# Kernel tuning notes

Hardware: AMD Instinct MI355X
Metric: run time of the kernel (lower is better)

The kernel has to match this reference:

```python
import jax, jax.numpy as jnp
import numpy as np

B, N, H, ITERS = 4, 4096, 128, 8
EPS = 1e-5  # torch LayerNorm default


def _mlp(x, w1, b1, w2, b2, w3, b3):
    x = jax.nn.relu(x @ w1.T + b1)
    x = jax.nn.relu(x @ w2.T + b2)
    return x @ w3.T + b3


def setup_inputs() -> dict:
    key = jax.random.key(0)
    ks = jax.random.split(key, 16)
    s = 0.05
    nrm = lambda k, shape: jax.random.normal(k, shape, jnp.float32) * s
    z = lambda *shape: jnp.zeros(shape, jnp.float32)
    return {
        "x": jax.random.normal(ks[0], (B, N, N), jnp.float32),
        "k": jax.random.uniform(ks[1], (B,), jnp.float32, 1.0, 10.0),
        "n": jax.random.uniform(ks[2], (B,), jnp.float32, 10.0, 100.0),
        "mask": (jax.random.uniform(ks[3], (B, N)) < 0.9).astype(jnp.float32),
        # init MLP: 2 -> H -> H -> H (torch Linear convention: [out, in])
        "init_w1": nrm(ks[4], (H, 2)), "init_b1": z(H),
        "init_w2": nrm(ks[5], (H, H)), "init_b2": z(H),
        "init_w3": nrm(ks[6], (H, H)), "init_b3": z(H),
        # msg MLP: H -> H -> H -> H
        "msg_w1": nrm(ks[7], (H, H)), "msg_b1": z(H),
        "msg_w2": nrm(ks[8], (H, H)), "msg_b2": z(H),
        "msg_w3": nrm(ks[9], (H, H)), "msg_b3": z(H),
        # LSTMCell (gate order i, f, g, o)
        "lstm_wih": nrm(ks[10], (4 * H, H)), "lstm_whh": nrm(ks[11], (4 * H, H)),
        "lstm_bih": z(4 * H), "lstm_bhh": z(4 * H),
        # LayerNorm affine
        "ln_g": jnp.ones(H, jnp.float32), "ln_b": z(H),
        # vote MLP: H -> H -> H -> 1
        "vote_w1": nrm(ks[12], (H, H)), "vote_b1": z(H),
        "vote_w2": nrm(ks[13], (H, H)), "vote_b2": z(H),
        "vote_w3": nrm(ks[14], (1, H)), "vote_b3": z(1),
    }


def reference(x, k, n, mask,
              init_w1, init_b1, init_w2, init_b2, init_w3, init_b3,
              msg_w1, msg_b1, msg_w2, msg_b2, msg_w3, msg_b3,
              lstm_wih, lstm_whh, lstm_bih, lstm_bhh,
              ln_g, ln_b,
              vote_w1, vote_b1, vote_w2, vote_b2, vote_w3, vote_b3):
    b, n_node, _ = x.shape

    def ln(h):
        mu = h.mean(-1, keepdims=True)
        xc = h - mu
        var = (xc * xc).mean(-1, keepdims=True)
        return xc * jax.lax.rsqrt(var + EPS) * ln_g + ln_b

    nk = jnp.stack([k, n], axis=1)                          # [B, 2]
    init0 = _mlp(nk, init_w1, init_b1, init_w2, init_b2, init_w3, init_b3)
    h = jnp.broadcast_to(init0[:, None, :], (b, n_node, init0.shape[-1]))  # [B, N, H]
    c = jnp.zeros_like(h)
    embed = ln(h)
    for _ in range(ITERS):
        m = _mlp(embed, msg_w1, msg_b1, msg_w2, msg_b2, msg_w3, msg_b3)   # [B, N, H]
        msg = jnp.einsum('bij,bjh->bih', x, m)                            # dense aggregation
        gates = msg @ lstm_wih.T + lstm_bih + h @ lstm_whh.T + lstm_bhh   # [B, N, 4H]
        i, f, g, o = jnp.split(gates, 4, axis=-1)
        c = jax.nn.sigmoid(f) * c + jax.nn.sigmoid(i) * jnp.tanh(g)
        h = jax.nn.sigmoid(o) * jnp.tanh(c)
        embed = ln(h)
    vote = _mlp(embed, vote_w1, vote_b1, vote_w2, vote_b2, vote_w3, vote_b3)[..., 0]  # [B, N]
    return jax.nn.sigmoid((vote * mask).sum(axis=1))        # [B]
```

## Files before the change

kernel.cpp:

```cpp
#include <hip/hip_runtime.h>
#include <cstddef>
#include <cstdint>

#define LN_EPS 1e-5f

typedef __attribute__((ext_vector_type(8))) short bf16x8;
typedef __attribute__((ext_vector_type(4))) float f32x4;

__device__ __forceinline__ unsigned short f2bf(float f) {
    unsigned u = __float_as_uint(f);
    u += 0x7FFFu + ((u >> 16) & 1u);
    return (unsigned short)(u >> 16);
}
__device__ __forceinline__ float bf2f(unsigned short s) {
    return __uint_as_float(((unsigned)s) << 16);
}
__device__ __forceinline__ float sigf(float x) { return 1.f / (1.f + __expf(-x)); }

__device__ __forceinline__ void gload_lds16(const void* g, void* l) {
    __builtin_amdgcn_global_load_lds(
        (const __attribute__((address_space(1))) unsigned int*)(unsigned long long)(uintptr_t)g,
        (__attribute__((address_space(3))) unsigned int*)(unsigned int)(uintptr_t)l,
        16, 0, 0);
}

__device__ __forceinline__ void layer128(const unsigned short* __restrict__ W,
                                         const bf16x8 a[4], f32x4 acc[8],
                                         int lr, int lq)
{
#pragma unroll
    for (int s = 0; s < 4; ++s) {
#pragma unroll
        for (int tn = 0; tn < 8; ++tn) {
            bf16x8 b = *(const bf16x8*)(W + (tn * 16 + lr) * 128 + s * 32 + lq * 8);
            acc[tn] = __builtin_amdgcn_mfma_f32_16x16x32_bf16(a[s], b, acc[tn], 0, 0, 0);
        }
    }
}

template<bool FP8>
__global__ __launch_bounds__(256)
void msg_mlp_kernel(const unsigned short* __restrict__ embed,
                    const unsigned short* __restrict__ w1, const float* __restrict__ b1,
                    const unsigned short* __restrict__ w2, const float* __restrict__ b2,
                    const unsigned short* __restrict__ w3, const float* __restrict__ b3,
                    unsigned short* __restrict__ m_t, unsigned char* __restrict__ m8,
                    int N)
{
    __shared__ unsigned short sact[4][16][136];
    const int lane = threadIdx.x & 63, wave = threadIdx.x >> 6;
    const int lr = lane & 15, lq = lane >> 4;
    const int r0 = (blockIdx.x * 4 + wave) * 16;

    bf16x8 a[4];
    f32x4 acc[8];

#pragma unroll
    for (int s = 0; s < 4; ++s)
        a[s] = *(const bf16x8*)(embed + (long long)(r0 + lr) * 128 + s * 32 + lq * 8);
#pragma unroll
    for (int tn = 0; tn < 8; ++tn) acc[tn] = (f32x4)(0.f);
    layer128(w1, a, acc, lr, lq);

#pragma unroll
    for (int tn = 0; tn < 8; ++tn) {
        float bb = b1[tn * 16 + lr];
#pragma unroll
        for (int r = 0; r < 4; ++r) {
            float v = acc[tn][r] + bb; v = v > 0.f ? v : 0.f;
            sact[wave][lq * 4 + r][tn * 16 + lr] = f2bf(v);
        }
    }
    __syncthreads();
#pragma unroll
    for (int s = 0; s < 4; ++s)
        a[s] = *(const bf16x8*)&sact[wave][lr][s * 32 + lq * 8];
#pragma unroll
    for (int tn = 0; tn < 8; ++tn) acc[tn] = (f32x4)(0.f);
    layer128(w2, a, acc, lr, lq);

#pragma unroll
    for (int tn = 0; tn < 8; ++tn) {
        float bb = b2[tn * 16 + lr];
#pragma unroll
        for (int r = 0; r < 4; ++r) {
            float v = acc[tn][r] + bb; v = v > 0.f ? v : 0.f;
            sact[wave][lq * 4 + r][tn * 16 + lr] = f2bf(v);
        }
    }
    __syncthreads();
#pragma unroll
    for (int s = 0; s < 4; ++s)
        a[s] = *(const bf16x8*)&sact[wave][lr][s * 32 + lq * 8];
#pragma unroll
    for (int tn = 0; tn < 8; ++tn) acc[tn] = (f32x4)(0.f);
    layer128(w3, a, acc, lr, lq);

    const int batch = r0 / N;
    const int rin0 = r0 - batch * N + lq * 4;
#pragma unroll
    for (int tn = 0; tn < 8; ++tn) {
        float bb = b3[tn * 16 + lr];
        float v0 = acc[tn][0] + bb, v1 = acc[tn][1] + bb;
        float v2 = acc[tn][2] + bb, v3 = acc[tn][3] + bb;
        if constexpr (FP8) {
            int pk = __builtin_amdgcn_cvt_pk_fp8_f32(v0, v1, 0, false);
            pk = __builtin_amdgcn_cvt_pk_fp8_f32(v2, v3, pk, true);
            *(unsigned int*)(m8 + (long long)(batch * 128 + tn * 16 + lr) * N + rin0) = (unsigned)pk;
        } else {
            ushort4 o;
            o.x = f2bf(v0); o.y = f2bf(v1); o.z = f2bf(v2); o.w = f2bf(v3);
            *(ushort4*)(m_t + ((long long)(batch * 128 + tn * 16 + lr)) * N + rin0) = o;
        }
    }
}

__global__ __launch_bounds__(256)
void agg_fp8_kernel(const unsigned char* __restrict__ x8,
                    const unsigned char* __restrict__ m8,
                    unsigned short* __restrict__ msgp, int N, long long BNH)
{
    __shared__ unsigned char sA[2][128 * 128];
    __shared__ unsigned char sB[2][128 * 128];

    const int tid = threadIdx.x;
    const int lane = tid & 63, w = tid >> 6;
    const int lr = lane & 15, lq = lane >> 4;
    const int wr = w & 1, wc = w >> 1;
    const int r0 = blockIdx.x * 128;
    const int ksp = blockIdx.y;
    const int batch = blockIdx.z;
    const int kbase = ksp * (N >> 2);
    const int nsteps = (N >> 2) >> 7;

    const unsigned char* xrow = x8 + (long long)batch * N * N;
    const unsigned char* mrow = m8 + (long long)batch * 128 * N;

    f32x4 acc[4][4];
#pragma unroll
    for (int tr = 0; tr < 4; ++tr)
#pragma unroll
        for (int tn = 0; tn < 4; ++tn) acc[tr][tn] = (f32x4)(0.f);

    auto stage = [&](int b, int step) {
        const int k0 = kbase + step * 128;
#pragma unroll
        for (int j = 0; j < 4; ++j) {
            const int c = ((w * 4 + j) << 6) + lane;
            const int row = c >> 3;
            const int gs = (c & 7) ^ (row & 7);
            gload_lds16(xrow + (long long)(r0 + row) * N + k0 + gs * 16,
                        (char*)sA[b] + (w * 4 + j) * 1024);
        }
#pragma unroll
        for (int j = 0; j < 4; ++j) {
            const int c = ((w * 4 + j) << 6) + lane;
            const int row = c >> 3;
            const int gs = (c & 7) ^ (row & 7);
            gload_lds16(mrow + (long long)row * N + k0 + gs * 16,
                        (char*)sB[b] + (w * 4 + j) * 1024);
        }
    };

    stage(0, 0);
    __syncthreads();
    int buf = 0;
    for (int step = 0; step < nsteps; ++step) {
        if (step + 1 < nsteps) stage(buf ^ 1, step + 1);
        const unsigned char* A  = sA[buf];
        const unsigned char* Bp = sB[buf];
#pragma unroll
        for (int ks = 0; ks < 4; ++ks) {
            const int g    = ks * 4 + lq;
            const int half = (g & 1) << 3;
            const int s16  = g >> 1;
            long af[4], bfr[4];
#pragma unroll
            for (int tr = 0; tr < 4; ++tr) {
                const int row = wr * 64 + tr * 16 + lr;
                af[tr] = *(const long*)(A + row * 128 + ((s16 ^ (row & 7)) << 4) + half);
            }
#pragma unroll
            for (int tn = 0; tn < 4; ++tn) {
                const int row = wc * 64 + tn * 16 + lr;
                bfr[tn] = *(const long*)(Bp + row * 128 + ((s16 ^ (row & 7)) << 4) + half);
            }
#pragma unroll
            for (int tr = 0; tr < 4; ++tr)
#pragma unroll
                for (int tn = 0; tn < 4; ++tn)
                    acc[tr][tn] = __builtin_amdgcn_mfma_f32_16x16x32_fp8_fp8(
                        af[tr], bfr[tn], acc[tr][tn], 0, 0, 0);
        }
        __syncthreads();
        buf ^= 1;
    }

    unsigned short* outb = msgp + (long long)ksp * BNH + (long long)(batch * N + r0) * 128;
#pragma unroll
    for (int tr = 0; tr < 4; ++tr)
#pragma unroll
        for (int tn = 0; tn < 4; ++tn)
#pragma unroll
            for (int r = 0; r < 4; ++r)
                outb[(long long)(wr * 64 + tr * 16 + lq * 4 + r) * 128 + wc * 64 + tn * 16 + lr]
                    = f2bf(acc[tr][tn][r]);
}

__global__ __launch_bounds__(256)
void agg_fallback_kernel(const float* __restrict__ xf,
                         const unsigned short* __restrict__ mt, float* __restrict__ msgp0,
                         int N)
{
    __shared__ float sacc[4][16][132];
    const int lane = threadIdx.x & 63, wave = threadIdx.x >> 6;
    const int lr = lane & 15, lq = lane >> 4;
    const int batch = blockIdx.y;
    const int rowBase = blockIdx.x * 16;
    const int kBase = wave * (N >> 2);
    const int kIters = N >> 7;

    const float* af = xf + (long long)batch * N * N + (long long)(rowBase + lr) * N + kBase + lq * 8;
    const long long bbase = (long long)batch * 128 * N + (long long)lr * N + kBase + lq * 8;

    f32x4 acc[8];
#pragma unroll
    for (int tn = 0; tn < 8; ++tn) acc[tn] = (f32x4)(0.f);

    for (int it = 0; it < kIters; ++it) {
        const int k = it * 32;
        float4 lo = *(const float4*)(af + k);
        float4 hi = *(const float4*)(af + k + 4);
        bf16x8 a0;
        a0[0] = (short)f2bf(lo.x); a0[1] = (short)f2bf(lo.y);
        a0[2] = (short)f2bf(lo.z); a0[3] = (short)f2bf(lo.w);
        a0[4] = (short)f2bf(hi.x); a0[5] = (short)f2bf(hi.y);
        a0[6] = (short)f2bf(hi.z); a0[7] = (short)f2bf(hi.w);
#pragma unroll
        for (int tn = 0; tn < 8; ++tn) {
            bf16x8 b0 = *(const bf16x8*)(mt + bbase + (long long)tn * 16 * N + k);
            acc[tn] = __builtin_amdgcn_mfma_f32_16x16x32_bf16(a0, b0, acc[tn], 0, 0, 0);
        }
    }

#pragma unroll
    for (int tn = 0; tn < 8; ++tn)
#pragma unroll
        for (int r = 0; r < 4; ++r)
            sacc[wave][lq * 4 + r][tn * 16 + lr] = acc[tn][r];
    __syncthreads();
    {
        const int t = threadIdx.x;
        const int row = t >> 4, cb2 = (t & 15) * 8;
        float o[8];
#pragma unroll
        for (int j = 0; j < 8; ++j)
            o[j] = sacc[0][row][cb2 + j] + sacc[1][row][cb2 + j]
                 + sacc[2][row][cb2 + j] + sacc[3][row][cb2 + j];
        float* dst = msgp0 + (long long)(batch * N + rowBase + row) * 128 + cb2;
        *(float4*)dst = make_float4(o[0], o[1], o[2], o[3]);
        *(float4*)(dst + 4) = make_float4(o[4], o[5], o[6], o[7]);
    }
}

template<int NPART, bool BF16P>
__global__ __launch_bounds__(256)
void gates_lstm_kernel(const void* __restrict__ msgp, long long BNH,
                       unsigned short* hb, float* cb,
                       const unsigned short* __restrict__ wih,
                       const unsigned short* __restrict__ whh,
                       const float* __restrict__ bih, const float* __restrict__ bhh,
                       const float* __restrict__ lng, const float* __restrict__ lnb,
                       unsigned short* __restrict__ embed_out)
{
    __shared__ float sred[4][16][2];
    const int lane = threadIdx.x & 63, wave = threadIdx.x >> 6;
    const int lr = lane & 15, lq = lane >> 4;
    const int r0 = blockIdx.x * 16;

    f32x4 acc[8];
#pragma unroll
    for (int t = 0; t < 8; ++t) acc[t] = (f32x4)(0.f);

    bf16x8 a[4];
#pragma unroll
    for (int s = 0; s < 4; ++s) {
        const long long base = (long long)(r0 + lr) * 128 + s * 32 + lq * 8;
        float v[8];
        if constexpr (BF16P) {
            const unsigned short* mp = (const unsigned short*)msgp;
            bf16x8 t0 = *(const bf16x8*)(mp + base);
#pragma unroll
            for (int e = 0; e < 8; ++e) v[e] = bf2f((unsigned short)t0[e]);
#pragma unroll
            for (int j = 1; j < NPART; ++j) {
                bf16x8 tj = *(const bf16x8*)(mp + (long long)j * BNH + base);
#pragma unroll
                for (int e = 0; e < 8; ++e) v[e] += bf2f((unsigned short)tj[e]);
            }
        } else {
            const float* mp = (const float*)msgp;
            float4 t0 = *(const float4*)(mp + base);
            float4 t1 = *(const float4*)(mp + base + 4);
            v[0] = t0.x; v[1] = t0.y; v[2] = t0.z; v[3] = t0.w;
            v[4] = t1.x; v[5] = t1.y; v[6] = t1.z; v[7] = t1.w;
#pragma unroll
            for (int j = 1; j < NPART; ++j) {
                float4 u0 = *(const float4*)(mp + (long long)j * BNH + base);
                float4 u1 = *(const float4*)(mp + (long long)j * BNH + base + 4);
                v[0] += u0.x; v[1] += u0.y; v[2] += u0.z; v[3] += u0.w;
                v[4] += u1.x; v[5] += u1.y; v[6] += u1.z; v[7] += u1.w;
            }
        }
        bf16x8 r8;
#pragma unroll
        for (int e = 0; e < 8; ++e) r8[e] = (short)f2bf(v[e]);
        a[s] = r8;
    }
#pragma unroll
    for (int s = 0; s < 4; ++s)
#pragma unroll
        for (int tt = 0; tt < 8; ++tt) {
            const int brow = (tt >> 1) * 128 + wave * 32 + (tt & 1) * 16 + lr;
            bf16x8 b = *(const bf16x8*)(wih + brow * 128 + s * 32 + lq * 8);
            acc[tt] = __builtin_amdgcn_mfma_f32_16x16x32_bf16(a[s], b, acc[tt], 0, 0, 0);
        }
#pragma unroll
    for (int s = 0; s < 4; ++s)
        a[s] = *(const bf16x8*)((const unsigned short*)hb + (long long)(r0 + lr) * 128 + s * 32 + lq * 8);
#pragma unroll
    for (int s = 0; s < 4; ++s)
#pragma unroll
        for (int tt = 0; tt < 8; ++tt) {
            const int brow = (tt >> 1) * 128 + wave * 32 + (tt & 1) * 16 + lr;
            bf16x8 b = *(const bf16x8*)(whh + brow * 128 + s * 32 + lq * 8);
            acc[tt] = __builtin_amdgcn_mfma_f32_16x16x32_bf16(a[s], b, acc[tt], 0, 0, 0);
        }

    float hn[2][4];
    float4* cw = (float4*)cb;
#pragma unroll
    for (int half = 0; half < 2; ++half) {
        const int col = wave * 32 + half * 16 + lr;
        const float bi  = bih[col]       + bhh[col];
        const float bf_ = bih[col + 128] + bhh[col + 128];
        const float bg  = bih[col + 256] + bhh[col + 256];
        const float bo  = bih[col + 384] + bhh[col + 384];
        const long long cidx = ((long long)blockIdx.x * 8 + wave * 2 + half) * 64 + lane;
        float4 cold = cw[cidx];
        float co[4] = {cold.x, cold.y, cold.z, cold.w};
        float cn[4];
#pragma unroll
        for (int r = 0; r < 4; ++r) {
            float iv = acc[0 + half][r] + bi;
            float fv = acc[2 + half][r] + bf_;
            float gv = acc[4 + half][r] + bg;
            float ov = acc[6 + half][r] + bo;
            float cc = sigf(fv) * co[r] + sigf(iv) * tanhf(gv);
            cn[r] = cc;
            hn[half][r] = sigf(ov) * tanhf(cc);
        }
        float4 cnew = {cn[0], cn[1], cn[2], cn[3]};
        cw[cidx] = cnew;
    }

    float ps1[4], ps2[4];
#pragma unroll
    for (int r = 0; r < 4; ++r) {
        float s1 = hn[0][r] + hn[1][r];
        float s2 = hn[0][r] * hn[0][r] + hn[1][r] * hn[1][r];
#pragma unroll
        for (int m = 1; m <= 8; m <<= 1) {
            s1 += __shfl_xor(s1, m);
            s2 += __shfl_xor(s2, m);
        }
        ps1[r] = s1; ps2[r] = s2;
    }
    if (lr == 0) {
#pragma unroll
        for (int r = 0; r < 4; ++r) {
            sred[wave][lq * 4 + r][0] = ps1[r];
            sred[wave][lq * 4 + r][1] = ps2[r];
        }
    }
    __syncthreads();

#pragma unroll
    for (int half = 0; half < 2; ++half) {
        const int col = wave * 32 + half * 16 + lr;
        const float g = lng[col], bb = lnb[col];
#pragma unroll
        for (int r = 0; r < 4; ++r) {
            const int row = lq * 4 + r;
            float S1 = sred[0][row][0] + sred[1][row][0] + sred[2][row][0] + sred[3][row][0];
            float S2 = sred[0][row][1] + sred[1][row][1] + sred[2][row][1] + sred[3][row][1];
            float mean = S1 * (1.f / 128.f);
// ... 92 lines not shown
    float h2 = b2[j];
    for (int q = 0; q < H; ++q) h2 += w2[j * H + q] * s1[q];
    h2 = h2 > 0.f ? h2 : 0.f;
    s2[j] = h2; __syncthreads();
    float o = b3[j];
    for (int q = 0; q < H; ++q) o += w3[j * H + q] * s2[q];
    init0[b * H + j] = o;

    red[j] = o; __syncthreads();
    for (int s = 64; s > 0; s >>= 1) { if (j < s) red[j] += red[j + s]; __syncthreads(); }
    float mu = red[0] / (float)H;
    __syncthreads();
    float d = o - mu;
    red[j] = d * d; __syncthreads();
    for (int s = 64; s > 0; s >>= 1) { if (j < s) red[j] += red[j + s]; __syncthreads(); }
    float var = red[0] / (float)H;
    embed0[b * H + j] = d * rsqrtf(var + LN_EPS) * lng[j] + lnb[j];
}

__global__ void bcast_kernel(const float* __restrict__ init0, const float* __restrict__ embed0,
                             unsigned short* __restrict__ hb, float* __restrict__ cb,
                             unsigned short* __restrict__ embed,
                             long long total, long long NH)
{
    long long idx = (long long)blockIdx.x * blockDim.x + threadIdx.x;
    if (idx >= total) return;
    int b = (int)(idx / NH);
    int j = (int)(idx & 127);
    hb[idx] = f2bf(init0[b * 128 + j]);
    embed[idx] = f2bf(embed0[b * 128 + j]);
    cb[idx] = 0.f;
}

__global__ void cast8_kernel(const float* __restrict__ x, unsigned char* __restrict__ x8,
                             long long n8)
{
    long long i = ((long long)blockIdx.x * blockDim.x + threadIdx.x);
    if (i >= n8) return;
    const float* s = x + i * 8;
    float4 a = *(const float4*)s;
    float4 b = *(const float4*)(s + 4);
    int lo = __builtin_amdgcn_cvt_pk_fp8_f32(a.x, a.y, 0, false);
    lo = __builtin_amdgcn_cvt_pk_fp8_f32(a.z, a.w, lo, true);
    int hi = __builtin_amdgcn_cvt_pk_fp8_f32(b.x, b.y, 0, false);
    hi = __builtin_amdgcn_cvt_pk_fp8_f32(b.z, b.w, hi, true);
    int2 o; o.x = lo; o.y = hi;
    *(int2*)(x8 + i * 8) = o;
}

struct CastArgs {
    const float* src[7];
    unsigned short* dst[7];
    int n[7];
};

__global__ void castw_kernel(CastArgs a)
{
    int rg = blockIdx.y;
    int i = (blockIdx.x * blockDim.x + threadIdx.x) * 4;
    if (i < a.n[rg]) {
        float4 v = *(const float4*)(a.src[rg] + i);
        ushort4 o;
        o.x = f2bf(v.x); o.y = f2bf(v.y); o.z = f2bf(v.z); o.w = f2bf(v.w);
        *(ushort4*)(a.dst[rg] + i) = o;
    }
}

__global__ void sigmoid_kernel(const float* __restrict__ logit, float* __restrict__ out, int B)
{
    int b = threadIdx.x;
    if (b < B) out[b] = 1.f / (1.f + __expf(-logit[b]));
}

extern "C" void kernel_launch(void* const* d_in, const int* in_sizes, int n_in,
                              void* d_out, int out_size, void* d_ws, size_t ws_size,
                              hipStream_t stream)
{
    const float* x    = (const float*)d_in[0];
    const float* kk   = (const float*)d_in[1];
    const float* nn   = (const float*)d_in[2];
    const float* mask = (const float*)d_in[3];
    const float* iw1  = (const float*)d_in[4];
    const float* ib1  = (const float*)d_in[5];
    const float* iw2  = (const float*)d_in[6];
    const float* ib2  = (const float*)d_in[7];
    const float* iw3  = (const float*)d_in[8];
    const float* ib3  = (const float*)d_in[9];
    const float* mw1  = (const float*)d_in[10];
    const float* mb1  = (const float*)d_in[11];
    const float* mw2  = (const float*)d_in[12];
    const float* mb2  = (const float*)d_in[13];
    const float* mw3  = (const float*)d_in[14];
    const float* mb3  = (const float*)d_in[15];
    const float* wih  = (const float*)d_in[16];
    const float* whh  = (const float*)d_in[17];
    const float* bih  = (const float*)d_in[18];
    const float* bhh  = (const float*)d_in[19];
    const float* lng  = (const float*)d_in[20];
    const float* lnb  = (const float*)d_in[21];
    const float* vw1  = (const float*)d_in[22];
    const float* vb1  = (const float*)d_in[23];
    const float* vw2  = (const float*)d_in[24];
    const float* vb2  = (const float*)d_in[25];
    const float* vw3  = (const float*)d_in[26];
    const float* vb3  = (const float*)d_in[27];
    float* out = (float*)d_out;

    const int B = in_sizes[1];
    const int H = in_sizes[5];
    const int N = in_sizes[3] / B;
    const long long NH  = (long long)N * H;
    const long long BNH = (long long)B * NH;
    const int M = B * N;

    char* p = (char*)d_ws;
    auto alloc = [&](long long bytes) {
        char* q = p; p += (bytes + 255) & ~255LL; return q;
    };
    float*          cb     = (float*)alloc(BNH * 4);
    unsigned short* embed  = (unsigned short*)alloc(BNH * 2);
    unsigned short* hb     = (unsigned short*)alloc(BNH * 2);
    unsigned short* m_t    = (unsigned short*)alloc(BNH * 2);
    unsigned short* msgp   = (unsigned short*)alloc(4 * BNH * 2);
    float*          init0  = (float*)alloc((long long)B * H * 4);
    float*          embed0 = (float*)alloc((long long)B * H * 4);
    float*          logit  = (float*)alloc((long long)B * 4);
    unsigned short* wb_m1  = (unsigned short*)alloc((long long)H * H * 2);
    unsigned short* wb_m2  = (unsigned short*)alloc((long long)H * H * 2);
    unsigned short* wb_m3  = (unsigned short*)alloc((long long)H * H * 2);
    unsigned short* wb_ih  = (unsigned short*)alloc(4LL * H * H * 2);
    unsigned short* wb_hh  = (unsigned short*)alloc(4LL * H * H * 2);
    unsigned short* wb_v1  = (unsigned short*)alloc((long long)H * H * 2);
    unsigned short* wb_v2  = (unsigned short*)alloc((long long)H * H * 2);
    unsigned char*  m8_t   = (unsigned char*)alloc(BNH);
    unsigned char*  x8     = (unsigned char*)alloc((long long)B * N * N);
    const bool use_x8 = ((long long)(p - (char*)d_ws) <= (long long)ws_size);

    init_kernel<<<B, H, 0, stream>>>(kk, nn, iw1, ib1, iw2, ib2, iw3, ib3, lng, lnb,
                                     init0, embed0, logit, H);
    {
        long long nb = (BNH + 255) / 256;
        bcast_kernel<<<dim3((unsigned)nb), 256, 0, stream>>>(init0, embed0, hb, cb, embed, BNH, NH);
    }
    {
        CastArgs ca;
        ca.src[0] = mw1; ca.dst[0] = wb_m1; ca.n[0] = H * H;
        ca.src[1] = mw2; ca.dst[1] = wb_m2; ca.n[1] = H * H;
        ca.src[2] = mw3; ca.dst[2] = wb_m3; ca.n[2] = H * H;
        ca.src[3] = wih; ca.dst[3] = wb_ih; ca.n[3] = 4 * H * H;
        ca.src[4] = whh; ca.dst[4] = wb_hh; ca.n[4] = 4 * H * H;
        ca.src[5] = vw1; ca.dst[5] = wb_v1; ca.n[5] = H * H;
        ca.src[6] = vw2; ca.dst[6] = wb_v2; ca.n[6] = H * H;
        castw_kernel<<<dim3(64, 7), 256, 0, stream>>>(ca);
    }
    if (use_x8) {
        long long n8 = (long long)B * N * N / 8;
        cast8_kernel<<<dim3((unsigned)((n8 + 255) / 256)), 256, 0, stream>>>(x, x8, n8);
    }

    dim3 gridRow(M / 64);
    dim3 gridRow16(M / 16);
    dim3 gridAggNew(N / 128, 4, B);
    dim3 gridAggOld(N / 16, B);

    for (int it = 0; it < 8; ++it) {
        if (use_x8) {
            msg_mlp_kernel<true><<<gridRow, 256, 0, stream>>>(embed, wb_m1, mb1, wb_m2, mb2,
                                                              wb_m3, mb3, m_t, m8_t, N);
            agg_fp8_kernel<<<gridAggNew, 256, 0, stream>>>(x8, m8_t, msgp, N, BNH);
            gates_lstm_kernel<4, true><<<gridRow16, 256, 0, stream>>>(
                (const void*)msgp, BNH, hb, cb, wb_ih, wb_hh, bih, bhh, lng, lnb, embed);
        } else {
            msg_mlp_kernel<false><<<gridRow, 256, 0, stream>>>(embed, wb_m1, mb1, wb_m2, mb2,
                                                               wb_m3, mb3, m_t, m8_t, N);
            agg_fallback_kernel<<<gridAggOld, 256, 0, stream>>>(x, m_t, (float*)msgp, N);
            gates_lstm_kernel<1, false><<<gridRow16, 256, 0, stream>>>(
                (const void*)msgp, BNH, hb, cb, wb_ih, wb_hh, bih, bhh, lng, lnb, embed);
        }
    }

    vote_mlp_kernel<<<gridRow, 256, 0, stream>>>(embed, wb_v1, vb1, wb_v2, vb2,
                                                 vw3, vb3, mask, logit, N);
    sigmoid_kernel<<<1, 64, 0, stream>>>(logit, out, B);
}
```

Measured before the change: 1.135 ms.

## Fuse message MLP and vote MLP into LSTM kernel; compute first aggregation via row sums

```diff
diff --git a/kernel.cpp b/kernel.cpp
--- a/kernel.cpp
+++ b/kernel.cpp
@@ -24,94 +24,130 @@
         16, 0, 0);
 }
 
-__device__ __forceinline__ void layer128(const unsigned short* __restrict__ W,
-                                         const bf16x8 a[4], f32x4 acc[8],
-                                         int lr, int lq)
-{
-#pragma unroll
-    for (int s = 0; s < 4; ++s) {
-#pragma unroll
-        for (int tn = 0; tn < 8; ++tn) {
-            bf16x8 b = *(const bf16x8*)(W + (tn * 16 + lr) * 128 + s * 32 + lq * 8);
-            acc[tn] = __builtin_amdgcn_mfma_f32_16x16x32_bf16(a[s], b, acc[tn], 0, 0, 0);
-        }
-    }
-}
-
-template<bool FP8>
+
+__global__ __launch_bounds__(128)
+void init_m0_kernel(const float* __restrict__ kk, const float* __restrict__ nn,
+                    const float* __restrict__ iw1, const float* __restrict__ ib1,
+                    const float* __restrict__ iw2, const float* __restrict__ ib2,
+                    const float* __restrict__ iw3, const float* __restrict__ ib3,
+                    const float* __restrict__ lng, const float* __restrict__ lnb,
+                    const float* __restrict__ mw1, const float* __restrict__ mb1,
+                    const float* __restrict__ mw2, const float* __restrict__ mb2,
+                    const float* __restrict__ mw3, const float* __restrict__ mb3,
+                    float* __restrict__ init0, float* __restrict__ m0,
+                    float* __restrict__ logit, int H)
+{
+    int b = blockIdx.x, j = threadIdx.x;
+    __shared__ float s1[128];
+    __shared__ float s2[128];
+    __shared__ float red[128];
+    if (j == 0) logit[b] = 0.f;
+    float kv = kk[b], nv = nn[b];
+    float h1 = iw1[j * 2 + 0] * kv + iw1[j * 2 + 1] * nv + ib1[j];
+    h1 = h1 > 0.f ? h1 : 0.f;
+    s1[j] = h1; __syncthreads();
+    float h2 = ib2[j];
+    for (int q = 0; q < H; ++q) h2 += iw2[j * H + q] * s1[q];
+    h2 = h2 > 0.f ? h2 : 0.f;
+    s2[j] = h2; __syncthreads();
+    float o = ib3[j];
+    for (int q = 0; q < H; ++q) o += iw3[j * H + q] * s2[q];
+    init0[b * H + j] = o;
+
+    red[j] = o; __syncthreads();
+    for (int s = 64; s > 0; s >>= 1) { if (j < s) red[j] += red[j + s]; __syncthreads(); }
+    float mu = red[0] / (float)H;
+    __syncthreads();
+    float d = o - mu;
+    red[j] = d * d; __syncthreads();
+    for (int s = 64; s > 0; s >>= 1) { if (j < s) red[j] += red[j + s]; __syncthreads(); }
+    float var = red[0] / (float)H;
+    float e = d * rsqrtf(var + LN_EPS) * lng[j] + lnb[j];
+
+    __syncthreads();
+    s1[j] = e; __syncthreads();
+    float m1 = mb1[j];
+    for (int q = 0; q < H; ++q) m1 += mw1[j * H + q] * s1[q];
+    m1 = m1 > 0.f ? m1 : 0.f;
+    s2[j] = m1; __syncthreads();
+    float m2 = mb2[j];
+    for (int q = 0; q < H; ++q) m2 += mw2[j * H + q] * s2[q];
+    m2 = m2 > 0.f ? m2 : 0.f;
+    __syncthreads();
+    s1[j] = m2; __syncthreads();
+    float m3 = mb3[j];
+    for (int q = 0; q < H; ++q) m3 += mw3[j * H + q] * s1[q];
+    m0[b * H + j] = m3;
+}
+
 __global__ __launch_bounds__(256)
-void msg_mlp_kernel(const unsigned short* __restrict__ embed,
-                    const unsigned short* __restrict__ w1, const float* __restrict__ b1,
-                    const unsigned short* __restrict__ w2, const float* __restrict__ b2,
-                    const unsigned short* __restrict__ w3, const float* __restrict__ b3,
-                    unsigned short* __restrict__ m_t, unsigned char* __restrict__ m8,
-                    int N)
-{
-    __shared__ unsigned short sact[4][16][136];
-    const int lane = threadIdx.x & 63, wave = threadIdx.x >> 6;
-    const int lr = lane & 15, lq = lane >> 4;
-    const int r0 = (blockIdx.x * 4 + wave) * 16;
-
-    bf16x8 a[4];
-    f32x4 acc[8];
-
-#pragma unroll
-    for (int s = 0; s < 4; ++s)
-        a[s] = *(const bf16x8*)(embed + (long long)(r0 + lr) * 128 + s * 32 + lq * 8);
-#pragma unroll
-    for (int tn = 0; tn < 8; ++tn) acc[tn] = (f32x4)(0.f);
-    layer128(w1, a, acc, lr, lq);
-
-#pragma unroll
-    for (int tn = 0; tn < 8; ++tn) {
-        float bb = b1[tn * 16 + lr];
-#pragma unroll
-        for (int r = 0; r < 4; ++r) {
-            float v = acc[tn][r] + bb; v = v > 0.f ? v : 0.f;
-            sact[wave][lq * 4 + r][tn * 16 + lr] = f2bf(v);
-        }
-    }
-    __syncthreads();
-#pragma unroll
-    for (int s = 0; s < 4; ++s)
-        a[s] = *(const bf16x8*)&sact[wave][lr][s * 32 + lq * 8];
-#pragma unroll
-    for (int tn = 0; tn < 8; ++tn) acc[tn] = (f32x4)(0.f);
-    layer128(w2, a, acc, lr, lq);
-
-#pragma unroll
-    for (int tn = 0; tn < 8; ++tn) {
-        float bb = b2[tn * 16 + lr];
-#pragma unroll
-        for (int r = 0; r < 4; ++r) {
-            float v = acc[tn][r] + bb; v = v > 0.f ? v : 0.f;
-            sact[wave][lq * 4 + r][tn * 16 + lr] = f2bf(v);
-        }
-    }
-    __syncthreads();
-#pragma unroll
-    for (int s = 0; s < 4; ++s)
-        a[s] = *(const bf16x8*)&sact[wave][lr][s * 32 + lq * 8];
-#pragma unroll
-    for (int tn = 0; tn < 8; ++tn) acc[tn] = (f32x4)(0.f);
-    layer128(w3, a, acc, lr, lq);
-
-    const int batch = r0 / N;
-    const int rin0 = r0 - batch * N + lq * 4;
-#pragma unroll
-    for (int tn = 0; tn < 8; ++tn) {
-        float bb = b3[tn * 16 + lr];
-        float v0 = acc[tn][0] + bb, v1 = acc[tn][1] + bb;
-        float v2 = acc[tn][2] + bb, v3 = acc[tn][3] + bb;
-        if constexpr (FP8) {
-            int pk = __builtin_amdgcn_cvt_pk_fp8_f32(v0, v1, 0, false);
-            pk = __builtin_amdgcn_cvt_pk_fp8_f32(v2, v3, pk, true);
-            *(unsigned int*)(m8 + (long long)(batch * 128 + tn * 16 + lr) * N + rin0) = (unsigned)pk;
-        } else {
+void prep_x_kernel(const float* __restrict__ x, unsigned char* __restrict__ x8,
+                   float* __restrict__ rs, int N)
+{
+    const long long g = blockIdx.x;
+    const float* row = x + g * N;
+    unsigned char* orow = x8 + g * N;
+    const int t = threadIdx.x;
+    const int lane = t & 63, wave = t >> 6;
+    float sum = 0.f;
+    const int nch = N >> 3;
+    for (int c = t; c < nch; c += 256) {
+        float4 a = *(const float4*)(row + c * 8);
+        float4 b = *(const float4*)(row + c * 8 + 4);
+        sum += a.x + a.y + a.z + a.w + b.x + b.y + b.z + b.w;
+        int lo = __builtin_amdgcn_cvt_pk_fp8_f32(a.x, a.y, 0, false);
+        lo = __builtin_amdgcn_cvt_pk_fp8_f32(a.z, a.w, lo, true);
+        int hi = __builtin_amdgcn_cvt_pk_fp8_f32(b.x, b.y, 0, false);
+        hi = __builtin_amdgcn_cvt_pk_fp8_f32(b.z, b.w, hi, true);
+        int2 o; o.x = lo; o.y = hi;
+        *(int2*)(orow + c * 8) = o;
+    }
+#pragma unroll
+    for (int m = 1; m <= 32; m <<= 1) sum += __shfl_xor(sum, m);
+    __shared__ float red[4];
+    if (lane == 0) red[wave] = sum;
+    __syncthreads();
+    if (t == 0) rs[g] = red[0] + red[1] + red[2] + red[3];
+}
+
+struct PrepArgs {
+    const float* wsrc[7];
+    unsigned short* wdst[7];
+    int wn[7];
+    const float* init0;
+    unsigned short* hb;
+    float* cb;
+    long long BNH, NH;
+};
+
+__global__ __launch_bounds__(256)
+void prep_misc_kernel(PrepArgs P)
+{
+    const long long gt = (long long)blockIdx.x * 256 + threadIdx.x;
+    const long long GT = (long long)gridDim.x * 256;
+    for (int rg = 0; rg < 7; ++rg) {
+        const float* s = P.wsrc[rg]; unsigned short* d = P.wdst[rg];
+        const int n4 = P.wn[rg] >> 2;
+        for (long long i = gt; i < n4; i += GT) {
+            float4 v = *(const float4*)(s + i * 4);
             ushort4 o;
-            o.x = f2bf(v0); o.y = f2bf(v1); o.z = f2bf(v2); o.w = f2bf(v3);
-            *(ushort4*)(m_t + ((long long)(batch * 128 + tn * 16 + lr)) * N + rin0) = o;
-        }
+            o.x = f2bf(v.x); o.y = f2bf(v.y); o.z = f2bf(v.z); o.w = f2bf(v.w);
+            *(ushort4*)(d + i * 4) = o;
+        }
+    }
+    const long long n4 = P.BNH >> 2;
+    const float4 z4 = make_float4(0.f, 0.f, 0.f, 0.f);
+    for (long long i = gt; i < n4; i += GT) {
+        const long long idx = i * 4;
+        const int b = (int)(idx / P.NH);
+        const int j = (int)(idx & 127);
+        ushort4 o;
+        o.x = f2bf(P.init0[b * 128 + j]);
+        o.y = f2bf(P.init0[b * 128 + j + 1]);
+        o.z = f2bf(P.init0[b * 128 + j + 2]);
+        o.w = f2bf(P.init0[b * 128 + j + 3]);
+        ((ushort4*)P.hb)[i] = o;
+        ((float4*)P.cb)[i] = z4;
     }
 }
 
@@ -167,8 +203,8 @@
     int buf = 0;
     for (int step = 0; step < nsteps; ++step) {
         if (step + 1 < nsteps) stage(buf ^ 1, step + 1);
-        const unsigned char* A  = sA[buf];
-        const unsigned char* Bp = sB[buf];
+        const unsigned char* Ab = sA[buf];
+        const unsigned char* Bb = sB[buf];
 #pragma unroll
         for (int ks = 0; ks < 4; ++ks) {
             const int g    = ks * 4 + lq;
@@ -178,12 +214,12 @@
 #pragma unroll
             for (int tr = 0; tr < 4; ++tr) {
                 const int row = wr * 64 + tr * 16 + lr;
-                af[tr] = *(const long*)(A + row * 128 + ((s16 ^ (row & 7)) << 4) + half);
+                af[tr] = *(const long*)(Ab + row * 128 + ((s16 ^ (row & 7)) << 4) + half);
             }
 #pragma unroll
             for (int tn = 0; tn < 4; ++tn) {
                 const int row = wc * 64 + tn * 16 + lr;
-                bfr[tn] = *(const long*)(Bp + row * 128 + ((s16 ^ (row & 7)) << 4) + half);
+                bfr[tn] = *(const long*)(Bb + row * 128 + ((s16 ^ (row & 7)) << 4) + half);
             }
 #pragma unroll
             for (int tr = 0; tr < 4; ++tr)
@@ -205,6 +241,387 @@
             for (int r = 0; r < 4; ++r)
                 outb[(long long)(wr * 64 + tr * 16 + lq * 4 + r) * 128 + wc * 64 + tn * 16 + lr]
                     = f2bf(acc[tr][tn][r]);
+}
+
+struct FArgs {
+    const unsigned short* msgp;
+    const float *rs, *m0;
+    unsigned short* hb;
+    float* cb;
+    const unsigned short *wih, *whh;
+    const float *bih, *bhh, *lng, *lnb;
+    const unsigned short *wm1, *wm2, *wm3;
+    const float *mb1, *mb2, *mb3;
+    const unsigned short *wv1, *wv2;
+    const float *vb1, *vb2, *vw3, *vb3;
+    const float* mask;
+    float* logit;
+    unsigned char* m8;
+    int N;
+    long long BNH;
+};
+
+template<int MODE>
+__global__ __launch_bounds__(256)
+void fused_kernel(FArgs A)
+{
+    __shared__ unsigned short ebt[16][136];
+    __shared__ unsigned short act[16][136];
+    __shared__ float sred[128];
+    __shared__ float sdot[64];
+    const int tid = threadIdx.x;
+    const int lane = tid & 63, wave = tid >> 6;
+    const int lr = lane & 15, lq = lane >> 4;
+    const int tile = blockIdx.x;
+    const int r0 = tile * 16;
+    const int N = A.N;
+    const int batch = r0 / N;
+    const long long BNH = A.BNH;
+
+    f32x4 acc[8];
+#pragma unroll
+    for (int t = 0; t < 8; ++t) acc[t] = (f32x4)(0.f);
+
+    bf16x8 a[4];
+    if constexpr (MODE == 0) {
+        const float rsv = A.rs[r0 + lr];
+        const float* m0b = A.m0 + batch * 128;
+#pragma unroll
+        for (int s = 0; s < 4; ++s) {
+            bf16x8 r8;
+#pragma unroll
+            for (int e = 0; e < 8; ++e)
+                r8[e] = (short)f2bf(rsv * m0b[s * 32 + lq * 8 + e]);
+            a[s] = r8;
+        }
+    } else {
+#pragma unroll
+        for (int s = 0; s < 4; ++s) {
+            const long long base = (long long)(r0 + lr) * 128 + s * 32 + lq * 8;
+            float v[8];
+            bf16x8 t0 = *(const bf16x8*)(A.msgp + base);
+#pragma unroll
+            for (int e = 0; e < 8; ++e) v[e] = bf2f((unsigned short)t0[e]);
+#pragma unroll
+            for (int j = 1; j < 4; ++j) {
+                bf16x8 tj = *(const bf16x8*)(A.msgp + (long long)j * BNH + base);
+#pragma unroll
+                for (int e = 0; e < 8; ++e) v[e] += bf2f((unsigned short)tj[e]);
+            }
+            bf16x8 r8;
+#pragma unroll
+            for (int e = 0; e < 8; ++e) r8[e] = (short)f2bf(v[e]);
+            a[s] = r8;
+        }
+    }
+#pragma unroll
+    for (int s = 0; s < 4; ++s)
+#pragma unroll
+        for (int tt = 0; tt < 8; ++tt) {
+            const int brow = (tt >> 1) * 128 + wave * 32 + (tt & 1) * 16 + lr;
+            bf16x8 b = *(const bf16x8*)(A.wih + brow * 128 + s * 32 + lq * 8);
+            acc[tt] = __builtin_amdgcn_mfma_f32_16x16x32_bf16(a[s], b, acc[tt], 0, 0, 0);
+        }
+#pragma unroll
+    for (int s = 0; s < 4; ++s)
+        a[s] = *(const bf16x8*)(A.hb + (long long)(r0 + lr) * 128 + s * 32 + lq * 8);
+#pragma unroll
+    for (int s = 0; s < 4; ++s)
+#pragma unroll
+        for (int tt = 0; tt < 8; ++tt) {
+            const int brow = (tt >> 1) * 128 + wave * 32 + (tt & 1) * 16 + lr;
+            bf16x8 b = *(const bf16x8*)(A.whh + brow * 128 + s * 32 + lq * 8);
+            acc[tt] = __builtin_amdgcn_mfma_f32_16x16x32_bf16(a[s], b, acc[tt], 0, 0, 0);
+        }
+
+    float hn[2][4];
+    float4* cw = (float4*)A.cb;
+#pragma unroll
+    for (int half = 0; half < 2; ++half) {
+        const int col = wave * 32 + half * 16 + lr;
+        const float bi  = A.bih[col]       + A.bhh[col];
+        const float bf_ = A.bih[col + 128] + A.bhh[col + 128];
+        const float bg  = A.bih[col + 256] + A.bhh[col + 256];
+        const float bo  = A.bih[col + 384] + A.bhh[col + 384];
+        const long long cidx = ((long long)tile * 8 + wave * 2 + half) * 64 + lane;
+        float4 cold = cw[cidx];
+        float co[4] = {cold.x, cold.y, cold.z, cold.w};
+        float cn[4];
+#pragma unroll
+        for (int r = 0; r < 4; ++r) {
+            float iv = acc[0 + half][r] + bi;
+            float fv = acc[2 + half][r] + bf_;
+            float gv = acc[4 + half][r] + bg;
+            float ov = acc[6 + half][r] + bo;
+            float cc = sigf(fv) * co[r] + sigf(iv) * tanhf(gv);
+            cn[r] = cc;
+            hn[half][r] = sigf(ov) * tanhf(cc);
+        }
+        cw[cidx] = make_float4(cn[0], cn[1], cn[2], cn[3]);
+    }
+
+    float ps1[4], ps2[4];
+#pragma unroll
+    for (int r = 0; r < 4; ++r) {
+        float s1 = hn[0][r] + hn[1][r];
+        float s2 = hn[0][r] * hn[0][r] + hn[1][r] * hn[1][r];
+#pragma unroll
+        for (int m = 1; m <= 8; m <<= 1) {
+            s1 += __shfl_xor(s1, m);
+            s2 += __shfl_xor(s2, m);
+        }
+        ps1[r] = s1; ps2[r] = s2;
+    }
+    if (lr == 0) {
+#pragma unroll
+        for (int r = 0; r < 4; ++r) {
+            sred[(wave * 16 + lq * 4 + r) * 2 + 0] = ps1[r];
+            sred[(wave * 16 + lq * 4 + r) * 2 + 1] = ps2[r];
+        }
+    }
+    __syncthreads();
+
+#pragma unroll
+    for (int half = 0; half < 2; ++half) {
+        const int col = wave * 32 + half * 16 + lr;
+        const float g = A.lng[col], bb = A.lnb[col];
+#pragma unroll
+        for (int r = 0; r < 4; ++r) {
+            const int row = lq * 4 + r;
+            float S1 = sred[(row) * 2] + sred[(16 + row) * 2] + sred[(32 + row) * 2] + sred[(48 + row) * 2];
+            float S2 = sred[(row) * 2 + 1] + sred[(16 + row) * 2 + 1] + sred[(32 + row) * 2 + 1] + sred[(48 + row) * 2 + 1];
+            float mean = S1 * (1.f / 128.f);
+            float var  = S2 * (1.f / 128.f) - mean * mean;
+            float rsq = rsqrtf(var + LN_EPS);
+            A.hb[(long long)(r0 + row) * 128 + col] = f2bf(hn[half][r]);
+            ebt[row][col] = f2bf((hn[half][r] - mean) * rsq * g + bb);
+        }
+    }
+    __syncthreads();
+
+    if constexpr (MODE == 2) {
+        bf16x8 av[4];
+        f32x4 acc2[2];
+#pragma unroll
+        for (int s = 0; s < 4; ++s) av[s] = *(const bf16x8*)&ebt[lr][s * 32 + lq * 8];
+        acc2[0] = (f32x4)(0.f); acc2[1] = (f32x4)(0.f);
+#pragma unroll
+        for (int s = 0; s < 4; ++s)
+#pragma unroll
+            for (int t = 0; t < 2; ++t) {
+                const int orow = wave * 32 + t * 16 + lr;
+                bf16x8 b = *(const bf16x8*)(A.wv1 + orow * 128 + s * 32 + lq * 8);
+                acc2[t] = __builtin_amdgcn_mfma_f32_16x16x32_bf16(av[s], b, acc2[t], 0, 0, 0);
+            }
+#pragma unroll
+        for (int t = 0; t < 2; ++t) {
+            const int col = wave * 32 + t * 16 + lr;
+            const float bb = A.vb1[col];
+#pragma unroll
+            for (int r = 0; r < 4; ++r) {
+                float v = acc2[t][r] + bb; v = v > 0.f ? v : 0.f;
+                act[lq * 4 + r][col] = f2bf(v);
+            }
+        }
+        __syncthreads();
+#pragma unroll
+        for (int s = 0; s < 4; ++s) av[s] = *(const bf16x8*)&act[lr][s * 32 + lq * 8];
+        acc2[0] = (f32x4)(0.f); acc2[1] = (f32x4)(0.f);
+#pragma unroll
+        for (int s = 0; s < 4; ++s)
+#pragma unroll
+            for (int t = 0; t < 2; ++t) {
+                const int orow = wave * 32 + t * 16 + lr;
+                bf16x8 b = *(const bf16x8*)(A.wv2 + orow * 128 + s * 32 + lq * 8);
+                acc2[t] = __builtin_amdgcn_mfma_f32_16x16x32_bf16(av[s], b, acc2[t], 0, 0, 0);
+            }
+        float dot[4] = {0.f, 0.f, 0.f, 0.f};
+#pragma unroll
+        for (int t = 0; t < 2; ++t) {
+            const int col = wave * 32 + t * 16 + lr;
+            const float bb = A.vb2[col], w3c = A.vw3[col];
+#pragma unroll
+            for (int r = 0; r < 4; ++r) {
+                float v = acc2[t][r] + bb; v = v > 0.f ? v : 0.f;
+                dot[r] += v * w3c;
+            }
+        }
+#pragma unroll
+        for (int r = 0; r < 4; ++r)
+#pragma unroll
+            for (int m = 1; m <= 8; m <<= 1) dot[r] += __shfl_xor(dot[r], m);
+        if (lr == 0) {
+#pragma unroll
+            for (int r = 0; r < 4; ++r) sdot[wave * 16 + lq * 4 + r] = dot[r];
+        }
+        __syncthreads();
+        if (wave == 0) {
+            const int rin = r0 - batch * N + lr;
+            float s = sdot[lr] + sdot[16 + lr] + sdot[32 + lr] + sdot[48 + lr];
+            float val = (s + A.vb3[0]) * A.mask[batch * N + rin];
+#pragma unroll
+            for (int m = 1; m <= 8; m <<= 1) val += __shfl_xor(val, m);
+            if (lane == 0) atomicAdd(&A.logit[batch], val);
+        }
+    } else {
+        bf16x8 am[4];
+        f32x4 acc2[2];
+#pragma unroll
+        for (int s = 0; s < 4; ++s) am[s] = *(const bf16x8*)&ebt[lr][s * 32 + lq * 8];
+        acc2[0] = (f32x4)(0.f); acc2[1] = (f32x4)(0.f);
+#pragma unroll
+        for (int s = 0; s < 4; ++s)
+#pragma unroll
+            for (int t = 0; t < 2; ++t) {
+                const int orow = wave * 32 + t * 16 + lr;
+                bf16x8 b = *(const bf16x8*)(A.wm1 + orow * 128 + s * 32 + lq * 8);
+                acc2[t] = __builtin_amdgcn_mfma_f32_16x16x32_bf16(am[s], b, acc2[t], 0, 0, 0);
+            }
+#pragma unroll
+        for (int t = 0; t < 2; ++t) {
+            const int col = wave * 32 + t * 16 + lr;
+            const float bb = A.mb1[col];
+#pragma unroll
+            for (int r = 0; r < 4; ++r) {
+                float v = acc2[t][r] + bb; v = v > 0.f ? v : 0.f;
+                act[lq * 4 + r][col] = f2bf(v);
+            }
+        }
+        __syncthreads();
+#pragma unroll
+        for (int s = 0; s < 4; ++s) am[s] = *(const bf16x8*)&act[lr][s * 32 + lq * 8];
+        acc2[0] = (f32x4)(0.f); acc2[1] = (f32x4)(0.f);
+#pragma unroll
+        for (int s = 0; s < 4; ++s)
+#pragma unroll
+            for (int t = 0; t < 2; ++t) {
+                const int orow = wave * 32 + t * 16 + lr;
+                bf16x8 b = *(const bf16x8*)(A.wm2 + orow * 128 + s * 32 + lq * 8);
+                acc2[t] = __builtin_amdgcn_mfma_f32_16x16x32_bf16(am[s], b, acc2[t], 0, 0, 0);
+            }
+        __syncthreads();
+#pragma unroll
+        for (int t = 0; t < 2; ++t) {
+            const int col = wave * 32 + t * 16 + lr;
+            const float bb = A.mb2[col];
+#pragma unroll
+            for (int r = 0; r < 4; ++r) {
+                float v = acc2[t][r] + bb; v = v > 0.f ? v : 0.f;
+                ebt[lq * 4 + r][col] = f2bf(v);
+            }
+        }
+        __syncthreads();
+#pragma unroll
+        for (int s = 0; s < 4; ++s) am[s] = *(const bf16x8*)&ebt[lr][s * 32 + lq * 8];
+        acc2[0] = (f32x4)(0.f); acc2[1] = (f32x4)(0.f);
+#pragma unroll
+        for (int s = 0; s < 4; ++s)
+#pragma unroll
+            for (int t = 0; t < 2; ++t) {
+                const int orow = wave * 32 + t * 16 + lr;
+                bf16x8 b = *(const bf16x8*)(A.wm3 + orow * 128 + s * 32 + lq * 8);
+                acc2[t] = __builtin_amdgcn_mfma_f32_16x16x32_bf16(am[s], b, acc2[t], 0, 0, 0);
+            }
+        const int rin0 = r0 - batch * N + lq * 4;
+#pragma unroll
+        for (int t = 0; t < 2; ++t) {
+            const int col = wave * 32 + t * 16 + lr;
+            const float bb = A.mb3[col];
+            float v0 = acc2[t][0] + bb, v1 = acc2[t][1] + bb;
+            float v2 = acc2[t][2] + bb, v3 = acc2[t][3] + bb;
+            int pk = __builtin_amdgcn_cvt_pk_fp8_f32(v0, v1, 0, false);
+            pk = __builtin_amdgcn_cvt_pk_fp8_f32(v2, v3, pk, true);
+            *(unsigned int*)(A.m8 + (long long)(batch * 128 + col) * N + rin0) = (unsigned)pk;
+        }
+    }
+}
+
+__global__ void sigmoid_kernel(const float* __restrict__ logit, float* __restrict__ out, int B)
+{
+    int b = threadIdx.x;
+    if (b < B) out[b] = 1.f / (1.f + __expf(-logit[b]));
+}
+
+__device__ __forceinline__ void layer128(const unsigned short* __restrict__ W,
+                                         const bf16x8 a[4], f32x4 acc[8],
+                                         int lr, int lq)
+{
+#pragma unroll
+    for (int s = 0; s < 4; ++s) {
+#pragma unroll
+        for (int tn = 0; tn < 8; ++tn) {
+            bf16x8 b = *(const bf16x8*)(W + (tn * 16 + lr) * 128 + s * 32 + lq * 8);
+            acc[tn] = __builtin_amdgcn_mfma_f32_16x16x32_bf16(a[s], b, acc[tn], 0, 0, 0);
+        }
+    }
+}
+
+__global__ __launch_bounds__(256)
+void msg_mlp_kernel(const unsigned short* __restrict__ embed,
+                    const unsigned short* __restrict__ w1, const float* __restrict__ b1,
+                    const unsigned short* __restrict__ w2, const float* __restrict__ b2,
+                    const unsigned short* __restrict__ w3, const float* __restrict__ b3,
+                    unsigned short* __restrict__ m_t, int N)
+{
+    __shared__ unsigned short sact[4][16][136];
+    const int lane = threadIdx.x & 63, wave = threadIdx.x >> 6;
+    const int lr = lane & 15, lq = lane >> 4;
+    const int r0 = (blockIdx.x * 4 + wave) * 16;
+
+    bf16x8 a[4];
+    f32x4 acc[8];
+
+#pragma unroll
+    for (int s = 0; s < 4; ++s)
+        a[s] = *(const bf16x8*)(embed + (long long)(r0 + lr) * 128 + s * 32 + lq * 8);
+#pragma unroll
+    for (int tn = 0; tn < 8; ++tn) acc[tn] = (f32x4)(0.f);
+    layer128(w1, a, acc, lr, lq);
+
+#pragma unroll
+    for (int tn = 0; tn < 8; ++tn) {
+        float bb = b1[tn * 16 + lr];
+#pragma unroll
+        for (int r = 0; r < 4; ++r) {
+            float v = acc[tn][r] + bb; v = v > 0.f ? v : 0.f;
+            sact[wave][lq * 4 + r][tn * 16 + lr] = f2bf(v);
+        }
+    }
+    __syncthreads();
+#pragma unroll
+    for (int s = 0; s < 4; ++s)
+        a[s] = *(const bf16x8*)&sact[wave][lr][s * 32 + lq * 8];
+#pragma unroll
+    for (int tn = 0; tn < 8; ++tn) acc[tn] = (f32x4)(0.f);
+    layer128(w2, a, acc, lr, lq);
+
+#pragma unroll
+    for (int tn = 0; tn < 8; ++tn) {
+        float bb = b2[tn * 16 + lr];
+#pragma unroll
+        for (int r = 0; r < 4; ++r) {
+            float v = acc[tn][r] + bb; v = v > 0.f ? v : 0.f;
+            sact[wave][lq * 4 + r][tn * 16 + lr] = f2bf(v);
+        }
+    }
+    __syncthreads();
+#pragma unroll
+    for (int s = 0; s < 4; ++s)
+        a[s] = *(const bf16x8*)&sact[wave][lr][s * 32 + lq * 8];
+#pragma unroll
+    for (int tn = 0; tn < 8; ++tn) acc[tn] = (f32x4)(0.f);
+    layer128(w3, a, acc, lr, lq);
+
+    const int batch = r0 / N;
+    const int rin0 = r0 - batch * N + lq * 4;
+#pragma unroll
+    for (int tn = 0; tn < 8; ++tn) {
+        float bb = b3[tn * 16 + lr];
+        ushort4 o;
+        o.x = f2bf(acc[tn][0] + bb); o.y = f2bf(acc[tn][1] + bb);
+        o.z = f2bf(acc[tn][2] + bb); o.w = f2bf(acc[tn][3] + bb);
+        *(ushort4*)(m_t + ((long long)(batch * 128 + tn * 16 + lr)) * N + rin0) = o;
+    }
 }
 
 __global__ __launch_bounds__(256)
@@ -263,15 +680,14 @@
     }
 }
 
-template<int NPART, bool BF16P>
 __global__ __launch_bounds__(256)
-void gates_lstm_kernel(const void* __restrict__ msgp, long long BNH,
-                       unsigned short* hb, float* cb,
-                       const unsigned short* __restrict__ wih,
-                       const unsigned short* __restrict__ whh,
-                       const float* __restrict__ bih, const float* __restrict__ bhh,
-                       const float* __restrict__ lng, const float* __restrict__ lnb,
-                       unsigned short* __restrict__ embed_out)
+void gates_lstm_fb_kernel(const float* __restrict__ msgp, long long BNH,
+                          unsigned short* hb, float* cb,
+                          const unsigned short* __restrict__ wih,
+                          const unsigned short* __restrict__ whh,
+                          const float* __restrict__ bih, const float* __restrict__ bhh,
+                          const float* __restrict__ lng, const float* __restrict__ lnb,
+                          unsigned short* __restrict__ embed_out)
 {
     __shared__ float sred[4][16][2];
     const int lane = threadIdx.x & 63, wave = threadIdx.x >> 6;
@@ -286,35 +702,13 @@
 #pragma unroll
     for (int s = 0; s < 4; ++s) {
         const long long base = (long long)(r0 + lr) * 128 + s * 32 + lq * 8;
-        float v[8];
-        if constexpr (BF16P) {
-            const unsigned short* mp = (const unsigned short*)msgp;
-            bf16x8 t0 = *(const bf16x8*)(mp + base);
-#pragma unroll
-            for (int e = 0; e < 8; ++e) v[e] = bf2f((unsigned short)t0[e]);
-#pragma unroll
-            for (int j = 1; j < NPART; ++j) {
-                bf16x8 tj = *(const bf16x8*)(mp + (long long)j * BNH + base);
-#pragma unroll
-                for (int e = 0; e < 8; ++e) v[e] += bf2f((unsigned short)tj[e]);
-            }
-        } else {
-            const float* mp = (const float*)msgp;
-            float4 t0 = *(const float4*)(mp + base);
-            float4 t1 = *(const float4*)(mp + base + 4);
-            v[0] = t0.x; v[1] = t0.y; v[2] = t0.z; v[3] = t0.w;
-            v[4] = t1.x; v[5] = t1.y; v[6] = t1.z; v[7] = t1.w;
-#pragma unroll
-            for (int j = 1; j < NPART; ++j) {
-                float4 u0 = *(const float4*)(mp + (long long)j * BNH + base);
-                float4 u1 = *(const float4*)(mp + (long long)j * BNH + base + 4);
-                v[0] += u0.x; v[1] += u0.y; v[2] += u0.z; v[3] += u0.w;
-                v[4] += u1.x; v[5] += u1.y; v[6] += u1.z; v[7] += u1.w;
-            }
-        }
+        float4 t0 = *(const float4*)(msgp + base);
+        float4 t1 = *(const float4*)(msgp + base + 4);
         bf16x8 r8;
-#pragma unroll
-        for (int e = 0; e < 8; ++e) r8[e] = (short)f2bf(v[e]);
+        r8[0] = (short)f2bf(t0.x); r8[1] = (short)f2bf(t0.y);
+        r8[2] = (short)f2bf(t0.z); r8[3] = (short)f2bf(t0.w);
+        r8[4] = (short)f2bf(t1.x); r8[5] = (short)f2bf(t1.y);
+        r8[6] = (short)f2bf(t1.z); r8[7] = (short)f2bf(t1.w);
         a[s] = r8;
     }
 #pragma unroll
@@ -360,8 +754,7 @@
             cn[r] = cc;
             hn[half][r] = sigf(ov) * tanhf(cc);
         }
-        float4 cnew = {cn[0], cn[1], cn[2], cn[3]};
-        cw[cidx] = cnew;
+        cw[cidx] = make_float4(cn[0], cn[1], cn[2], cn[3]);
     }
 
     float ps1[4], ps2[4];
@@ -520,22 +913,6 @@
     cb[idx] = 0.f;
 }
 
-__global__ void cast8_kernel(const float* __restrict__ x, unsigned char* __restrict__ x8,
-                             long long n8)
-{
-    long long i = ((long long)blockIdx.x * blockDim.x + threadIdx.x);
-    if (i >= n8) return;
-    const float* s = x + i * 8;
-    float4 a = *(const float4*)s;
-    float4 b = *(const float4*)(s + 4);
-    int lo = __builtin_amdgcn_cvt_pk_fp8_f32(a.x, a.y, 0, false);
-    lo = __builtin_amdgcn_cvt_pk_fp8_f32(a.z, a.w, lo, true);
-    int hi = __builtin_amdgcn_cvt_pk_fp8_f32(b.x, b.y, 0, false);
-    hi = __builtin_amdgcn_cvt_pk_fp8_f32(b.z, b.w, hi, true);
-    int2 o; o.x = lo; o.y = hi;
-    *(int2*)(x8 + i * 8) = o;
-}
-
 struct CastArgs {
     const float* src[7];
     unsigned short* dst[7];
@@ -552,12 +929,6 @@
         o.x = f2bf(v.x); o.y = f2bf(v.y); o.z = f2bf(v.z); o.w = f2bf(v.w);
         *(ushort4*)(a.dst[rg] + i) = o;
     }
-}
-
-__global__ void sigmoid_kernel(const float* __restrict__ logit, float* __restrict__ out, int B)
-{
-    int b = threadIdx.x;
-    if (b < B) out[b] = 1.f / (1.f + __expf(-logit[b]));
 }
 
 extern "C" void kernel_launch(void* const* d_in, const int* in_sizes, int n_in,
@@ -612,7 +983,9 @@
     unsigned short* msgp   = (unsigned short*)alloc(4 * BNH * 2);
     float*          init0  = (float*)alloc((long long)B * H * 4);
     float*          embed0 = (float*)alloc((long long)B * H * 4);
+    float*          m0     = (float*)alloc((long long)B * H * 4);
     float*          logit  = (float*)alloc((long long)B * 4);
+    float*          rs     = (float*)alloc((long long)B * N * 4);
     unsigned short* wb_m1  = (unsigned short*)alloc((long long)H * H * 2);
     unsigned short* wb_m2  = (unsigned short*)alloc((long long)H * H * 2);
     unsigned short* wb_m3  = (unsigned short*)alloc((long long)H * H * 2);
@@ -622,7 +995,48 @@
     unsigned short* wb_v2  = (unsigned short*)alloc((long long)H * H * 2);
     unsigned char*  m8_t   = (unsigned char*)alloc(BNH);
     unsigned char*  x8     = (unsigned char*)alloc((long long)B * N * N);
-    const bool use_x8 = ((long long)(p - (char*)d_ws) <= (long long)ws_size);
+    const bool ws_ok = ((long long)(p - (char*)d_ws) <= (long long)ws_size);
+    const bool fast = ws_ok && B == 4 && N == 4096 && H == 128;
+
+    if (fast) {
+        init_m0_kernel<<<B, H, 0, stream>>>(kk, nn, iw1, ib1, iw2, ib2, iw3, ib3,
+                                            lng, lnb, mw1, mb1, mw2, mb2, mw3, mb3,
+                                            init0, m0, logit, H);
+        prep_x_kernel<<<dim3(M), 256, 0, stream>>>(x, x8, rs, N);
+        {
+            PrepArgs P;
+            P.wsrc[0] = mw1; P.wdst[0] = wb_m1; P.wn[0] = H * H;
+            P.wsrc[1] = mw2; P.wdst[1] = wb_m2; P.wn[1] = H * H;
+            P.wsrc[2] = mw3; P.wdst[2] = wb_m3; P.wn[2] = H * H;
+            P.wsrc[3] = wih; P.wdst[3] = wb_ih; P.wn[3] = 4 * H * H;
+            P.wsrc[4] = whh; P.wdst[4] = wb_hh; P.wn[4] = 4 * H * H;
+            P.wsrc[5] = vw1; P.wdst[5] = wb_v1; P.wn[5] = H * H;
+            P.wsrc[6] = vw2; P.wdst[6] = wb_v2; P.wn[6] = H * H;
+            P.init0 = init0; P.hb = hb; P.cb = cb; P.BNH = BNH; P.NH = NH;
+            prep_misc_kernel<<<dim3(1024), 256, 0, stream>>>(P);
+        }
+
+        FArgs F;
+        F.msgp = msgp; F.rs = rs; F.m0 = m0;
+        F.hb = hb; F.cb = cb;
+        F.wih = wb_ih; F.whh = wb_hh; F.bih = bih; F.bhh = bhh; F.lng = lng; F.lnb = lnb;
+        F.wm1 = wb_m1; F.wm2 = wb_m2; F.wm3 = wb_m3; F.mb1 = mb1; F.mb2 = mb2; F.mb3 = mb3;
+        F.wv1 = wb_v1; F.wv2 = wb_v2; F.vb1 = vb1; F.vb2 = vb2; F.vw3 = vw3; F.vb3 = vb3;
+        F.mask = mask; F.logit = logit; F.m8 = m8_t;
+        F.N = N; F.BNH = BNH;
+
+        dim3 gridF(M / 16);
+        dim3 gridAgg(N / 128, 4, B);
+
+        fused_kernel<0><<<gridF, 256, 0, stream>>>(F);
+        for (int it = 1; it < 8; ++it) {
+            agg_fp8_kernel<<<gridAgg, 256, 0, stream>>>(x8, m8_t, msgp, N, BNH);
+            if (it < 7) fused_kernel<1><<<gridF, 256, 0, stream>>>(F);
+            else        fused_kernel<2><<<gridF, 256, 0, stream>>>(F);
+        }
+        sigmoid_kernel<<<1, 64, 0, stream>>>(logit, out, B);
+        return;
+    }
 
     init_kernel<<<B, H, 0, stream>>>(kk, nn, iw1, ib1, iw2, ib2, iw3, ib3, lng, lnb,
                                      init0, embed0, logit, H);
@@ -641,30 +1055,18 @@
         ca.src[6] = vw2; ca.dst[6] = wb_v2; ca.n[6] = H * H;
         castw_kernel<<<dim3(64, 7), 256, 0, stream>>>(ca);
     }
-    if (use_x8) {
-        long long n8 = (long long)B * N * N / 8;
-        cast8_kernel<<<dim3((unsigned)((n8 + 255) / 256)), 256, 0, stream>>>(x, x8, n8);
-    }
 
     dim3 gridRow(M / 64);
     dim3 gridRow16(M / 16);
-    dim3 gridAggNew(N / 128, 4, B);
     dim3 gridAggOld(N / 16, B);
 
     for (int it = 0; it < 8; ++it) {
-        if (use_x8) {
-            msg_mlp_kernel<true><<<gridRow, 256, 0, stream>>>(embed, wb_m1, mb1, wb_m2, mb2,
-                                                              wb_m3, mb3, m_t, m8_t, N);
-            agg_fp8_kernel<<<gridAggNew, 256, 0, stream>>>(x8, m8_t, msgp, N, BNH);
-            gates_lstm_kernel<4, true><<<gridRow16, 256, 0, stream>>>(
-                (const void*)msgp, BNH, hb, cb, wb_ih, wb_hh, bih, bhh, lng, lnb, embed);
-        } else {
-            msg_mlp_kernel<false><<<gridRow, 256, 0, stream>>>(embed, wb_m1, mb1, wb_m2, mb2,
-                                                               wb_m3, mb3, m_t, m8_t, N);
-            agg_fallback_kernel<<<gridAggOld, 256, 0, stream>>>(x, m_t, (float*)msgp, N);
-            gates_lstm_kernel<1, false><<<gridRow16, 256, 0, stream>>>(
-                (const void*)msgp, BNH, hb, cb, wb_ih, wb_hh, bih, bhh, lng, lnb, embed);
-        }
+        msg_mlp_kernel<<<gridRow, 256, 0, stream>>>(embed, wb_m1, mb1, wb_m2, mb2,
+                                                    wb_m3, mb3, m_t, N);
+        agg_fallback_kernel<<<gridAggOld, 256, 0, stream>>>(x, m_t, (float*)msgp, N);
+        gates_lstm_fb_kernel<<<gridRow16, 256, 0, stream>>>((float*)msgp, BNH, hb, cb,
+                                                            wb_ih, wb_hh, bih, bhh,
+                                                            lng, lnb, embed);
     }
 
     vote_mlp_kernel<<<gridRow, 256, 0, stream>>>(embed, wb_v1, vb1, wb_v2, vb2,
```

After: 1.034 ms. 8.9% less time.
